# Kernel tuning notes

Hardware: AMD Instinct MI355X
Metric: run time of the kernel (lower is better)

## Reference

```python
import jax, jax.numpy as jnp
import numpy as np

N_NODES = 100000


def _graph_conv(x, W, b, src, dst, n_nodes):
    # DGL GraphConv, norm='both', weight applied before aggregation (in>out).
    E = src.shape[0]
    ones = jnp.ones((E,), dtype=x.dtype)
    out_deg = jax.ops.segment_sum(ones, src, num_segments=n_nodes)
    in_deg = jax.ops.segment_sum(ones, dst, num_segments=n_nodes)
    out_norm = jnp.clip(out_deg, 1.0, None) ** -0.5  # [N]
    in_norm = jnp.clip(in_deg, 1.0, None) ** -0.5    # [N]
    h = (x * out_norm[:, None]) @ W                  # [N, out] dense GEMM first
    msg = h[src]                                     # gather  [E, out]
    agg = jax.ops.segment_sum(msg, dst, num_segments=n_nodes)  # scatter-add
    return agg * in_norm[:, None] + b


def setup_inputs() -> dict:
    key = jax.random.key(0)
    k1, k2, k3, k4, k5 = jax.random.split(key, 5)
    E = 1600000
    features = jax.random.normal(k1, (N_NODES, 128), dtype=jnp.float32)
    src = jax.random.randint(k2, (E,), 0, N_NODES, dtype=jnp.int64)
    dst = jax.random.randint(k3, (E,), 0, N_NODES, dtype=jnp.int64)
    W1 = jax.random.normal(k4, (128, 64), dtype=jnp.float32) * (1.0 / np.sqrt(128))
    b1 = jnp.zeros((64,), dtype=jnp.float32)
    W2 = jax.random.normal(k5, (64, 32), dtype=jnp.float32) * (1.0 / np.sqrt(64))
    b2 = jnp.zeros((32,), dtype=jnp.float32)
    return {"features": features, "src": src, "dst": dst,
            "W1": W1, "b1": b1, "W2": W2, "b2": b2}


def reference(features, src, dst, W1, b1, W2, b2):
    x = jax.nn.relu(_graph_conv(features, W1, b1, src, dst, N_NODES))
    x = _graph_conv(x, W2, b2, src, dst, N_NODES)
    return x
```

## Files before the change

kernel.cpp:

```cpp
#include <hip/hip_runtime.h>
#include <hip/hip_bf16.h>


#define BSH 7
#define BNODES 128
#define SRCMASK 0x1FFFF
#define CAP 2560
#define CHUNK 4096

__device__ __forceinline__ unsigned short f2bf(float f) {
    unsigned int u = __float_as_uint(f);
    return (unsigned short)((u + 0x7FFFu + ((u >> 16) & 1u)) >> 16);
}

__device__ __forceinline__ float bflo(unsigned int u) {
    return __uint_as_float(u << 16);
}
__device__ __forceinline__ float bfhi(unsigned int u) {
    return __uint_as_float(u & 0xFFFF0000u);
}

__global__ __launch_bounds__(1024) void k_place(const int* __restrict__ src,
        const int* __restrict__ dst, int* __restrict__ ebuf,
        unsigned char* __restrict__ sbuf, int* __restrict__ offs,
        int* __restrict__ soffs, int E) {
    __shared__ int lh[800], s[800];
    int t = threadIdx.x;
    int e0 = blockIdx.x * CHUNK;
    int e1 = min(e0 + CHUNK, E);
    if (t < 800) lh[t] = 0;
    __syncthreads();
    for (int i = e0 + t; i < e1; i += 1024) {
        atomicAdd(&lh[dst[i] >> BSH], 0x10000);
        atomicAdd(&lh[src[i] >> BSH], 1);
    }
    __syncthreads();
    if (t < 800) s[t] = lh[t];
    __syncthreads();
    for (int o = 1; o < 800; o <<= 1) {
        int u = (t < 800 && t >= o) ? s[t - o] : 0;
        __syncthreads();
        if (t < 800) s[t] += u;
        __syncthreads();
    }
    int obase = blockIdx.x * 801;
    if (t < 800) {
        int incl = s[t], c = lh[t];
        int bd = (incl >> 16) - (c >> 16);
        int bs = (incl & 0xFFFF) - (c & 0xFFFF);
        offs[obase + t] = bd;
        soffs[obase + t] = bs;
        s[t] = (bd << 16) | bs;
    }
    if (t == 0) { offs[obase + 800] = e1 - e0; soffs[obase + 800] = e1 - e0; }
    __syncthreads();
    for (int i = e0 + t; i < e1; i += 1024) {
        int sv = src[i], d = dst[i];
        int pd = atomicAdd(&s[d >> BSH], 0x10000) >> 16;
        ebuf[e0 + pd] = sv | ((d & (BNODES - 1)) << 17);
        int ps = atomicAdd(&s[sv >> BSH], 1) & 0xFFFF;
        sbuf[e0 + ps] = (unsigned char)(sv & (BNODES - 1));
    }
}

__global__ __launch_bounds__(1024) void k_sort2(const int* __restrict__ ebuf,
        const unsigned char* __restrict__ sbuf, const int* __restrict__ offs,
        const int* __restrict__ soffs, int* __restrict__ csrc,
        int* __restrict__ ostart, int* __restrict__ oend,
        float* __restrict__ nI, float* __restrict__ nO, int n, int NBLK) {
    __shared__ int cnt[BNODES], cur[BNODES], s[BNODES], scnt[BNODES];
    __shared__ int segst[400], segen[400], sst[400], sen[400];
    int t = threadIdx.x, b = blockIdx.x;
    if (t < NBLK) {
        segst[t] = t * CHUNK + offs[t * 801 + b];
        segen[t] = t * CHUNK + offs[t * 801 + b + 1];
        sst[t]   = t * CHUNK + soffs[t * 801 + b];
        sen[t]   = t * CHUNK + soffs[t * 801 + b + 1];
    }
    if (t < BNODES) { cnt[t] = 0; scnt[t] = 0; }
    __syncthreads();
    int grp = t >> 3, ln = t & 7;
    for (int sg = grp; sg < NBLK; sg += 128) {
        int en = segen[sg];
        for (int i = segst[sg] + ln; i < en; i += 8)
            atomicAdd(&cnt[ebuf[i] >> 17], 1);
        int en2 = sen[sg];
        for (int i = sst[sg] + ln; i < en2; i += 8)
            atomicAdd(&scnt[sbuf[i]], 1);
    }
    __syncthreads();
    if (t < BNODES) s[t] = cnt[t];
    __syncthreads();
    for (int o = 1; o < BNODES; o <<= 1) {
        int u = (t < BNODES && t >= o) ? s[t - o] : 0;
        __syncthreads();
        if (t < BNODES) s[t] += u;
        __syncthreads();
    }
    if (t < BNODES) {
        int e0 = b * CAP;
        int st = e0 + s[t] - cnt[t];
        cur[t] = st;
        int g = b * BNODES + t;
        if (g < n) {
            ostart[g] = st;
            oend[g] = e0 + s[t];
            nI[g] = rsqrtf(fmaxf((float)cnt[t], 1.0f));
            nO[g] = rsqrtf(fmaxf((float)scnt[t], 1.0f));
        }
    }
    __syncthreads();
    for (int sg = grp; sg < NBLK; sg += 128) {
        int en = segen[sg];
        for (int i = segst[sg] + ln; i < en; i += 8) {
            int p = ebuf[i];
            int pos = atomicAdd(&cur[p >> 17], 1);
            csrc[pos] = p & SRCMASK;
        }
    }
}

__global__ __launch_bounds__(256) void k_gemm1(const float* __restrict__ x,
                        const float* __restrict__ W1, const float* __restrict__ nO,
                        unsigned short* __restrict__ h1, int n) {
    __shared__ float sX[64 * 132];
    __shared__ float sW[128 * 64];
    const int t = threadIdx.x;
    {
        const float4* W4 = (const float4*)W1;
        float4* sW4 = (float4*)sW;
#pragma unroll
        for (int i = 0; i < 8; i++) sW4[t + 256 * i] = W4[t + 256 * i];
    }
    const int rowbase = blockIdx.x * 64;
    {
        const float4* x4 = (const float4*)x;
        float4* sX4 = (float4*)sX;
#pragma unroll
        for (int i = 0; i < 8; i++) {
            int f = t + 256 * i;
            int row = f >> 5, kc = f & 31;
            int grow = rowbase + row;
            float4 v = make_float4(0.f, 0.f, 0.f, 0.f);
            if (grow < n) v = x4[(size_t)grow * 32 + kc];
            sX4[row * 33 + kc] = v;
        }
    }
    __syncthreads();
    const int lane = t & 63, wv = t >> 6;
    const int rg = lane >> 2, cg = lane & 3;
    const int c0 = wv * 16 + cg * 4;
    float acc[4][4] = {};
    for (int kk = 0; kk < 128; kk += 4) {
        float xr[4][4], wr[4][4];
#pragma unroll
        for (int i = 0; i < 4; i++)
            *(float4*)xr[i] = *(const float4*)&sX[(rg + 16 * i) * 132 + kk];
#pragma unroll
        for (int j = 0; j < 4; j++)
            *(float4*)wr[j] = *(const float4*)&sW[(kk + j) * 64 + c0];
#pragma unroll
        for (int j = 0; j < 4; j++)
#pragma unroll
            for (int i = 0; i < 4; i++)
#pragma unroll
                for (int c = 0; c < 4; c++)
                    acc[i][c] = fmaf(xr[i][j], wr[j][c], acc[i][c]);
    }
#pragma unroll
    for (int i = 0; i < 4; i++) {
        int grow = rowbase + rg + 16 * i;
        if (grow < n) {
            float nf = nO[grow];
            ushort4 o;
            o.x = f2bf(acc[i][0] * nf); o.y = f2bf(acc[i][1] * nf);
            o.z = f2bf(acc[i][2] * nf); o.w = f2bf(acc[i][3] * nf);
            *(ushort4*)&h1[(size_t)grow * 64 + c0] = o;
        }
    }
}

__global__ void k_agg64(const unsigned short* __restrict__ h,
                        const int* __restrict__ csrc,
                        const int* __restrict__ ostart, const int* __restrict__ oend,
                        const float* __restrict__ nI, const float* __restrict__ b1,
                        float* __restrict__ x2, int n) {
    int node = blockIdx.x * 4 + (threadIdx.x >> 6);
    int lane = threadIdx.x & 63;
    if (node >= n) return;
    int s0 = ostart[node], s1 = oend[node];
    int sub = lane >> 3;
    int c8 = (lane & 7) * 8;
    float a[8] = {}, d[8] = {};
    int e = s0;
    for (; e + 15 < s1; e += 16) {
        int p0 = csrc[e + sub];
        int p1 = csrc[e + 8 + sub];
        uint4 u0 = *(const uint4*)&h[(size_t)p0 * 64 + c8];
        uint4 u1 = *(const uint4*)&h[(size_t)p1 * 64 + c8];
        a[0] += bflo(u0.x); a[1] += bfhi(u0.x);
        a[2] += bflo(u0.y); a[3] += bfhi(u0.y);
        a[4] += bflo(u0.z); a[5] += bfhi(u0.z);
        a[6] += bflo(u0.w); a[7] += bfhi(u0.w);
        d[0] += bflo(u1.x); d[1] += bfhi(u1.x);
        d[2] += bflo(u1.y); d[3] += bfhi(u1.y);
        d[4] += bflo(u1.z); d[5] += bfhi(u1.z);
        d[6] += bflo(u1.w); d[7] += bfhi(u1.w);
    }
    for (; e < s1; e += 8) {
        if (e + sub < s1) {
            int p = csrc[e + sub];
            uint4 u = *(const uint4*)&h[(size_t)p * 64 + c8];
            a[0] += bflo(u.x); a[1] += bfhi(u.x);
            a[2] += bflo(u.y); a[3] += bfhi(u.y);
            a[4] += bflo(u.z); a[5] += bfhi(u.z);
            a[6] += bflo(u.w); a[7] += bfhi(u.w);
        }
    }
#pragma unroll
    for (int i = 0; i < 8; i++) a[i] += d[i];
#pragma unroll
    for (int i = 0; i < 8; i++) {
        a[i] += __shfl(a[i], lane ^ 8, 64);
        a[i] += __shfl(a[i], lane ^ 16, 64);
        a[i] += __shfl(a[i], lane ^ 32, 64);
    }
    if (sub == 0) {
        float ni = nI[node];
        float4 o0, o1;
        o0.x = fmaxf(fmaf(a[0], ni, b1[c8 + 0]), 0.f);
        o0.y = fmaxf(fmaf(a[1], ni, b1[c8 + 1]), 0.f);
        o0.z = fmaxf(fmaf(a[2], ni, b1[c8 + 2]), 0.f);
        o0.w = fmaxf(fmaf(a[3], ni, b1[c8 + 3]), 0.f);
        o1.x = fmaxf(fmaf(a[4], ni, b1[c8 + 4]), 0.f);
        o1.y = fmaxf(fmaf(a[5], ni, b1[c8 + 5]), 0.f);
        o1.z = fmaxf(fmaf(a[6], ni, b1[c8 + 6]), 0.f);
        o1.w = fmaxf(fmaf(a[7], ni, b1[c8 + 7]), 0.f);
        *(float4*)&x2[(size_t)node * 64 + c8] = o0;
        *(float4*)&x2[(size_t)node * 64 + c8 + 4] = o1;
    }
}

__global__ __launch_bounds__(256) void k_gemm2(const float* __restrict__ x2,
                        const float* __restrict__ W2, const float* __restrict__ nO,
                        unsigned short* __restrict__ h2, int n) {
    __shared__ float sX[128 * 68];
    __shared__ float sW[64 * 32];
    const int t = threadIdx.x;
    {
        const float4* W4 = (const float4*)W2;
        float4* sW4 = (float4*)sW;
#pragma unroll
        for (int i = 0; i < 2; i++) sW4[t + 256 * i] = W4[t + 256 * i];
    }
    const int rowbase = blockIdx.x * 128;
    {
        const float4* x4 = (const float4*)x2;
        float4* sX4 = (float4*)sX;
#pragma unroll
        for (int i = 0; i < 8; i++) {
            int f = t + 256 * i;
            int row = f >> 4, kc = f & 15;
            int grow = rowbase + row;
            float4 v = make_float4(0.f, 0.f, 0.f, 0.f);
            if (grow < n) v = x4[(size_t)grow * 16 + kc];
            sX4[row * 17 + kc] = v;
        }
    }
    __syncthreads();
    const int lane = t & 63, wv = t >> 6;
    const int whalf = wv >> 1, chalf = wv & 1;
    const int rg = lane >> 2, cg = lane & 3;
    const int c0 = chalf * 16 + cg * 4;
    const int rloc = whalf * 64 + rg;
    float acc[4][4] = {};
    for (int kk = 0; kk < 64; kk += 4) {
        float xr[4][4], wr[4][4];
#pragma unroll
        for (int i = 0; i < 4; i++)
            *(float4*)xr[i] = *(const float4*)&sX[(rloc + 16 * i) * 68 + kk];
#pragma unroll
        for (int j = 0; j < 4; j++)
            *(float4*)wr[j] = *(const float4*)&sW[(kk + j) * 32 + c0];
#pragma unroll
        for (int j = 0; j < 4; j++)
#pragma unroll
            for (int i = 0; i < 4; i++)
#pragma unroll
                for (int c = 0; c < 4; c++)
                    acc[i][c] = fmaf(xr[i][j], wr[j][c], acc[i][c]);
    }
#pragma unroll
    for (int i = 0; i < 4; i++) {
        int grow = rowbase + rloc + 16 * i;
        if (grow < n) {
            float nf = nO[grow];
            ushort4 o;
            o.x = f2bf(acc[i][0] * nf); o.y = f2bf(acc[i][1] * nf);
            o.z = f2bf(acc[i][2] * nf); o.w = f2bf(acc[i][3] * nf);
            *(ushort4*)&h2[(size_t)grow * 32 + c0] = o;
        }
    }
}

__global__ void k_agg32(const unsigned short* __restrict__ h,
                        const int* __restrict__ csrc,
                        const int* __restrict__ ostart, const int* __restrict__ oend,
                        const float* __restrict__ nI, const float* __restrict__ b2,
                        float* __restrict__ out, int n) {
    int node = blockIdx.x * 4 + (threadIdx.x >> 6);
    int lane = threadIdx.x & 63;
    if (node >= n) return;
    int s0 = ostart[node], s1 = oend[node];
    int sub = lane >> 2;
    int c8 = (lane & 3) * 8;
    float a[8] = {};
    int e = s0;
    for (; e + 15 < s1; e += 16) {
        int p = csrc[e + sub];
        uint4 u = *(const uint4*)&h[(size_t)p * 32 + c8];
        a[0] += bflo(u.x); a[1] += bfhi(u.x);
        a[2] += bflo(u.y); a[3] += bfhi(u.y);
        a[4] += bflo(u.z); a[5] += bfhi(u.z);
        a[6] += bflo(u.w); a[7] += bfhi(u.w);
    }
    for (; e < s1; e += 16) {
        if (e + sub < s1) {
            int p = csrc[e + sub];
            uint4 u = *(const uint4*)&h[(size_t)p * 32 + c8];
            a[0] += bflo(u.x); a[1] += bfhi(u.x);
            a[2] += bflo(u.y); a[3] += bfhi(u.y);
            a[4] += bflo(u.z); a[5] += bfhi(u.z);
            a[6] += bflo(u.w); a[7] += bfhi(u.w);
        }
    }
#pragma unroll
    for (int i = 0; i < 8; i++) {
        a[i] += __shfl(a[i], lane ^ 4, 64);
        a[i] += __shfl(a[i], lane ^ 8, 64);
        a[i] += __shfl(a[i], lane ^ 16, 64);
        a[i] += __shfl(a[i], lane ^ 32, 64);
    }
    if (sub == 0) {
        float ni = nI[node];
        float4 o0, o1;
        o0.x = fmaf(a[0], ni, b2[c8 + 0]);
        o0.y = fmaf(a[1], ni, b2[c8 + 1]);
        o0.z = fmaf(a[2], ni, b2[c8 + 2]);
        o0.w = fmaf(a[3], ni, b2[c8 + 3]);
        o1.x = fmaf(a[4], ni, b2[c8 + 4]);
        o1.y = fmaf(a[5], ni, b2[c8 + 5]);
        o1.z = fmaf(a[6], ni, b2[c8 + 6]);
        o1.w = fmaf(a[7], ni, b2[c8 + 7]);
        *(float4*)&out[(size_t)node * 32 + c8] = o0;
        *(float4*)&out[(size_t)node * 32 + c8 + 4] = o1;
    }
}

extern "C" void kernel_launch(void* const* d_in, const int* in_sizes, int n_in,
                              void* d_out, int out_size, void* d_ws, size_t ws_size,
                              hipStream_t stream) {
    const float* x   = (const float*)d_in[0];
    const int*   src = (const int*)d_in[1];
    const int*   dst = (const int*)d_in[2];
    const float* W1  = (const float*)d_in[3];
    const float* b1  = (const float*)d_in[4];
    const float* W2  = (const float*)d_in[5];
    const float* b2  = (const float*)d_in[6];
    float* out = (float*)d_out;

    const int N = in_sizes[0] / 128;
    const int E = in_sizes[1];
    const int NB = (N + BNODES - 1) / BNODES;
    const int NBLK = (E + CHUNK - 1) / CHUNK;

    char* wsb = (char*)d_ws;
    float* nO     = (float*)wsb;  wsb += (size_t)N * 4;
    float* nI     = (float*)wsb;  wsb += (size_t)N * 4;
    int*   ostart = (int*)wsb;    wsb += (size_t)N * 4;
    int*   oend   = (int*)wsb;    wsb += (size_t)N * 4;
    int*   csrc   = (int*)wsb;    wsb += (size_t)NB * CAP * 4;
    int*   offs   = (int*)wsb;    wsb += (size_t)NBLK * 801 * 4;
    unsigned short* h1 = (unsigned short*)wsb;
                                  wsb += (size_t)N * 64 * 2;
    float* x2     = (float*)wsb;  wsb += (size_t)N * 64 * 4;
    unsigned short* h2 = h1;
    int*   ebuf   = (int*)x2;
    unsigned char* sbuf = (unsigned char*)(ebuf) + (size_t)E * 4;
    int*   soffs  = (int*)(sbuf + (size_t)E);

    k_place<<<NBLK, 1024, 0, stream>>>(src, dst, ebuf, sbuf, offs, soffs, E);
    k_sort2<<<NB, 1024, 0, stream>>>(ebuf, sbuf, offs, soffs, csrc,
                                     ostart, oend, nI, nO, N, NBLK);

    k_gemm1<<<(N + 63) / 64, 256, 0, stream>>>(x, W1, nO, h1, N);
    k_agg64<<<(N + 3) / 4, 256, 0, stream>>>(h1, csrc, ostart, oend, nI, b1, x2, N);

    k_gemm2<<<(N + 127) / 128, 256, 0, stream>>>(x2, W2, nO, h2, N);
    k_agg32<<<(N + 3) / 4, 256, 0, stream>>>(h2, csrc, ostart, oend, nI, b2, out, N);
}
```

Measured before the change: 293.7 us.

## Split layer-1 features into four column slabs for cache-friendly aggregation

Gemm1 now writes h1 as four planar 16-column bf16 slabs instead of interleaved 64-wide rows. The layer-1 aggregation is split into four passes, one per slab, so each gathered working set (~3.2MB) fits in cache rather than the full 12.8MB table. Each wave handles 8 nodes with 16 edges in flight, and x2 is stored slab-major with gemm2 reading it accordingly. In exchange, the edge index lists are read four times and more shuffle reductions are done per node.

```diff
diff --git a/kernel.cpp b/kernel.cpp
--- a/kernel.cpp
+++ b/kernel.cpp
@@ -167,6 +167,7 @@
                 for (int c = 0; c < 4; c++)
                     acc[i][c] = fmaf(xr[i][j], wr[j][c], acc[i][c]);
     }
+    const size_t pl = (size_t)n * 16;
 #pragma unroll
     for (int i = 0; i < 4; i++) {
         int grow = rowbase + rg + 16 * i;
@@ -175,69 +176,64 @@
             ushort4 o;
             o.x = f2bf(acc[i][0] * nf); o.y = f2bf(acc[i][1] * nf);
             o.z = f2bf(acc[i][2] * nf); o.w = f2bf(acc[i][3] * nf);
-            *(ushort4*)&h1[(size_t)grow * 64 + c0] = o;
-        }
-    }
-}
-
-__global__ void k_agg64(const unsigned short* __restrict__ h,
-                        const int* __restrict__ csrc,
-                        const int* __restrict__ ostart, const int* __restrict__ oend,
-                        const float* __restrict__ nI, const float* __restrict__ b1,
-                        float* __restrict__ x2, int n) {
-    int node = blockIdx.x * 4 + (threadIdx.x >> 6);
-    int lane = threadIdx.x & 63;
-    if (node >= n) return;
-    int s0 = ostart[node], s1 = oend[node];
-    int sub = lane >> 3;
-    int c8 = (lane & 7) * 8;
-    float a[8] = {}, d[8] = {};
-    int e = s0;
-    for (; e + 15 < s1; e += 16) {
-        int p0 = csrc[e + sub];
-        int p1 = csrc[e + 8 + sub];
-        uint4 u0 = *(const uint4*)&h[(size_t)p0 * 64 + c8];
-        uint4 u1 = *(const uint4*)&h[(size_t)p1 * 64 + c8];
-        a[0] += bflo(u0.x); a[1] += bfhi(u0.x);
-        a[2] += bflo(u0.y); a[3] += bfhi(u0.y);
-        a[4] += bflo(u0.z); a[5] += bfhi(u0.z);
-        a[6] += bflo(u0.w); a[7] += bfhi(u0.w);
-        d[0] += bflo(u1.x); d[1] += bfhi(u1.x);
-        d[2] += bflo(u1.y); d[3] += bfhi(u1.y);
-        d[4] += bflo(u1.z); d[5] += bfhi(u1.z);
-        d[6] += bflo(u1.w); d[7] += bfhi(u1.w);
-    }
-    for (; e < s1; e += 8) {
-        if (e + sub < s1) {
-            int p = csrc[e + sub];
-            uint4 u = *(const uint4*)&h[(size_t)p * 64 + c8];
-            a[0] += bflo(u.x); a[1] += bfhi(u.x);
-            a[2] += bflo(u.y); a[3] += bfhi(u.y);
-            a[4] += bflo(u.z); a[5] += bfhi(u.z);
-            a[6] += bflo(u.w); a[7] += bfhi(u.w);
-        }
-    }
-#pragma unroll
-    for (int i = 0; i < 8; i++) a[i] += d[i];
-#pragma unroll
-    for (int i = 0; i < 8; i++) {
-        a[i] += __shfl(a[i], lane ^ 8, 64);
-        a[i] += __shfl(a[i], lane ^ 16, 64);
-        a[i] += __shfl(a[i], lane ^ 32, 64);
-    }
-    if (sub == 0) {
-        float ni = nI[node];
-        float4 o0, o1;
-        o0.x = fmaxf(fmaf(a[0], ni, b1[c8 + 0]), 0.f);
-        o0.y = fmaxf(fmaf(a[1], ni, b1[c8 + 1]), 0.f);
-        o0.z = fmaxf(fmaf(a[2], ni, b1[c8 + 2]), 0.f);
-        o0.w = fmaxf(fmaf(a[3], ni, b1[c8 + 3]), 0.f);
-        o1.x = fmaxf(fmaf(a[4], ni, b1[c8 + 4]), 0.f);
-        o1.y = fmaxf(fmaf(a[5], ni, b1[c8 + 5]), 0.f);
-        o1.z = fmaxf(fmaf(a[6], ni, b1[c8 + 6]), 0.f);
-        o1.w = fmaxf(fmaf(a[7], ni, b1[c8 + 7]), 0.f);
-        *(float4*)&x2[(size_t)node * 64 + c8] = o0;
-        *(float4*)&x2[(size_t)node * 64 + c8 + 4] = o1;
+            *(ushort4*)&h1[(size_t)wv * pl + (size_t)grow * 16 + cg * 4] = o;
+        }
+    }
+}
+
+__global__ __launch_bounds__(256) void k_agg64s2(const unsigned short* __restrict__ h,
+        const int* __restrict__ csrc, const int* __restrict__ ostart,
+        const int* __restrict__ oend, const float* __restrict__ nI,
+        const float* __restrict__ b1, float* __restrict__ x2, int n) {
+    const int s  = blockIdx.x & 3;
+    const int nb = blockIdx.x >> 2;
+    const int wid = threadIdx.x >> 6, lane = threadIdx.x & 63;
+    const int node0 = nb * 32 + wid * 8;
+    if (node0 >= n) return;
+    const int sub = lane >> 2;
+    const int cl = lane & 3;
+    const uint2* hs = (const uint2*)(h + (size_t)s * n * 16);
+    float* x2s = x2 + (size_t)s * n * 16;
+    const float4 bb = *(const float4*)&b1[s * 16 + cl * 4];
+    int pre = min(node0 + (lane & 7), n - 1);
+    int sA = ostart[pre], sB = oend[pre];
+#pragma unroll
+    for (int g = 0; g < 8; g++) {
+        int node = node0 + g;
+        if (node >= n) break;
+        int s0 = __shfl(sA, g, 64), s1 = __shfl(sB, g, 64);
+        float a0 = 0.f, a1 = 0.f, a2 = 0.f, a3 = 0.f;
+        for (int e = s0 + sub; e < s1; e += 16) {
+            int p = csrc[e];
+            uint2 u = hs[(size_t)p * 4 + cl];
+            a0 += bflo(u.x); a1 += bfhi(u.x);
+            a2 += bflo(u.y); a3 += bfhi(u.y);
+        }
+        a0 += __shfl(a0, lane ^ 4, 64);
+        a1 += __shfl(a1, lane ^ 4, 64);
+        a2 += __shfl(a2, lane ^ 4, 64);
+        a3 += __shfl(a3, lane ^ 4, 64);
+        a0 += __shfl(a0, lane ^ 8, 64);
+        a1 += __shfl(a1, lane ^ 8, 64);
+        a2 += __shfl(a2, lane ^ 8, 64);
+        a3 += __shfl(a3, lane ^ 8, 64);
+        a0 += __shfl(a0, lane ^ 16, 64);
+        a1 += __shfl(a1, lane ^ 16, 64);
+        a2 += __shfl(a2, lane ^ 16, 64);
+        a3 += __shfl(a3, lane ^ 16, 64);
+        a0 += __shfl(a0, lane ^ 32, 64);
+        a1 += __shfl(a1, lane ^ 32, 64);
+        a2 += __shfl(a2, lane ^ 32, 64);
+        a3 += __shfl(a3, lane ^ 32, 64);
+        if (sub == 0) {
+            float ni = nI[node];
+            float4 o;
+            o.x = fmaxf(fmaf(a0, ni, bb.x), 0.f);
+            o.y = fmaxf(fmaf(a1, ni, bb.y), 0.f);
+            o.z = fmaxf(fmaf(a2, ni, bb.z), 0.f);
+            o.w = fmaxf(fmaf(a3, ni, bb.w), 0.f);
+            *(float4*)&x2s[(size_t)node * 16 + cl * 4] = o;
+        }
     }
 }
 
@@ -254,6 +250,7 @@
         for (int i = 0; i < 2; i++) sW4[t + 256 * i] = W4[t + 256 * i];
     }
     const int rowbase = blockIdx.x * 128;
+    const size_t n4 = (size_t)n * 4;
     {
         const float4* x4 = (const float4*)x2;
         float4* sX4 = (float4*)sX;
@@ -263,7 +260,8 @@
             int row = f >> 4, kc = f & 15;
             int grow = rowbase + row;
             float4 v = make_float4(0.f, 0.f, 0.f, 0.f);
-            if (grow < n) v = x4[(size_t)grow * 16 + kc];
+            if (grow < n)
+                v = x4[(size_t)(kc >> 2) * n4 + (size_t)grow * 4 + (kc & 3)];
             sX4[row * 17 + kc] = v;
         }
     }
@@ -394,7 +392,8 @@
                                      ostart, oend, nI, nO, N, NBLK);
 
     k_gemm1<<<(N + 63) / 64, 256, 0, stream>>>(x, W1, nO, h1, N);
-    k_agg64<<<(N + 3) / 4, 256, 0, stream>>>(h1, csrc, ostart, oend, nI, b1, x2, N);
+    k_agg64s2<<<((N + 31) / 32) * 4, 256, 0, stream>>>(h1, csrc, ostart, oend,
+                                                       nI, b1, x2, N);
 
     k_gemm2<<<(N + 127) / 128, 256, 0, stream>>>(x2, W2, nO, h2, N);
     k_agg32<<<(N + 3) / 4, 256, 0, stream>>>(h2, csrc, ostart, oend, nI, b2, out, N);
```

Measured after the change: 333.2 us. 1.13x slower.

## Fuse layer-2 GEMM into layer-1 aggregation epilogue

Applied to the files above, without the earlier changes.

The first aggregation kernel now applies bias and ReLU, then multiplies each node's 64-wide row by W2 (held transposed in shared memory) with a shuffle reduction, and writes the bf16 h2 directly. This removes the fp32 x2 intermediate write and read and one kernel launch. In exchange every 4-node block reloads W2 into shared memory, which adds a barrier and extra shuffles per node. The workspace layout is reshuffled so that h2 aliases the sort scratch buffer.

```diff
diff --git a/kernel.cpp b/kernel.cpp
--- a/kernel.cpp
+++ b/kernel.cpp
@@ -180,17 +180,28 @@
     }
 }
 
-__global__ void k_agg64(const unsigned short* __restrict__ h,
-                        const int* __restrict__ csrc,
-                        const int* __restrict__ ostart, const int* __restrict__ oend,
-                        const float* __restrict__ nI, const float* __restrict__ b1,
-                        float* __restrict__ x2, int n) {
+__global__ __launch_bounds__(256) void k_agg64g2(const unsigned short* __restrict__ h,
+        const int* __restrict__ csrc,
+        const int* __restrict__ ostart, const int* __restrict__ oend,
+        const float* __restrict__ nI, const float* __restrict__ nO,
+        const float* __restrict__ b1, const float* __restrict__ W2,
+        unsigned short* __restrict__ h2, int n) {
+    __shared__ float sWT[32 * 68];
+    {
+        int t = threadIdx.x;
+        for (int i = t; i < 2048; i += 256) {
+            int cc = i & 31, k = i >> 5;
+            sWT[cc * 68 + k] = W2[(size_t)k * 32 + cc];
+        }
+    }
+    __syncthreads();
     int node = blockIdx.x * 4 + (threadIdx.x >> 6);
     int lane = threadIdx.x & 63;
     if (node >= n) return;
     int s0 = ostart[node], s1 = oend[node];
     int sub = lane >> 3;
-    int c8 = (lane & 7) * 8;
+    int q = lane & 7;
+    int c8 = q * 8;
     float a[8] = {}, d[8] = {};
     int e = s0;
     for (; e + 15 < s1; e += 16) {
@@ -225,81 +236,40 @@
         a[i] += __shfl(a[i], lane ^ 16, 64);
         a[i] += __shfl(a[i], lane ^ 32, 64);
     }
-    if (sub == 0) {
-        float ni = nI[node];
-        float4 o0, o1;
-        o0.x = fmaxf(fmaf(a[0], ni, b1[c8 + 0]), 0.f);
-        o0.y = fmaxf(fmaf(a[1], ni, b1[c8 + 1]), 0.f);
-        o0.z = fmaxf(fmaf(a[2], ni, b1[c8 + 2]), 0.f);
-        o0.w = fmaxf(fmaf(a[3], ni, b1[c8 + 3]), 0.f);
-        o1.x = fmaxf(fmaf(a[4], ni, b1[c8 + 4]), 0.f);
-        o1.y = fmaxf(fmaf(a[5], ni, b1[c8 + 5]), 0.f);
-        o1.z = fmaxf(fmaf(a[6], ni, b1[c8 + 6]), 0.f);
-        o1.w = fmaxf(fmaf(a[7], ni, b1[c8 + 7]), 0.f);
-        *(float4*)&x2[(size_t)node * 64 + c8] = o0;
-        *(float4*)&x2[(size_t)node * 64 + c8 + 4] = o1;
-    }
-}
-
-__global__ __launch_bounds__(256) void k_gemm2(const float* __restrict__ x2,
-                        const float* __restrict__ W2, const float* __restrict__ nO,
-                        unsigned short* __restrict__ h2, int n) {
-    __shared__ float sX[128 * 68];
-    __shared__ float sW[64 * 32];
-    const int t = threadIdx.x;
-    {
-        const float4* W4 = (const float4*)W2;
-        float4* sW4 = (float4*)sW;
-#pragma unroll
-        for (int i = 0; i < 2; i++) sW4[t + 256 * i] = W4[t + 256 * i];
-    }
-    const int rowbase = blockIdx.x * 128;
-    {
-        const float4* x4 = (const float4*)x2;
-        float4* sX4 = (float4*)sX;
-#pragma unroll
-        for (int i = 0; i < 8; i++) {
-            int f = t + 256 * i;
-            int row = f >> 4, kc = f & 15;
-            int grow = rowbase + row;
-            float4 v = make_float4(0.f, 0.f, 0.f, 0.f);
-            if (grow < n) v = x4[(size_t)grow * 16 + kc];
-            sX4[row * 17 + kc] = v;
-        }
-    }
-    __syncthreads();
-    const int lane = t & 63, wv = t >> 6;
-    const int whalf = wv >> 1, chalf = wv & 1;
-    const int rg = lane >> 2, cg = lane & 3;
-    const int c0 = chalf * 16 + cg * 4;
-    const int rloc = whalf * 64 + rg;
-    float acc[4][4] = {};
-    for (int kk = 0; kk < 64; kk += 4) {
-        float xr[4][4], wr[4][4];
-#pragma unroll
-        for (int i = 0; i < 4; i++)
-            *(float4*)xr[i] = *(const float4*)&sX[(rloc + 16 * i) * 68 + kk];
-#pragma unroll
-        for (int j = 0; j < 4; j++)
-            *(float4*)wr[j] = *(const float4*)&sW[(kk + j) * 32 + c0];
-#pragma unroll
-        for (int j = 0; j < 4; j++)
-#pragma unroll
-            for (int i = 0; i < 4; i++)
-#pragma unroll
-                for (int c = 0; c < 4; c++)
-                    acc[i][c] = fmaf(xr[i][j], wr[j][c], acc[i][c]);
-    }
-#pragma unroll
-    for (int i = 0; i < 4; i++) {
-        int grow = rowbase + rloc + 16 * i;
-        if (grow < n) {
-            float nf = nO[grow];
-            ushort4 o;
-            o.x = f2bf(acc[i][0] * nf); o.y = f2bf(acc[i][1] * nf);
-            o.z = f2bf(acc[i][2] * nf); o.w = f2bf(acc[i][3] * nf);
-            *(ushort4*)&h2[(size_t)grow * 32 + c0] = o;
-        }
+    float ni = nI[node];
+    float v[8];
+#pragma unroll
+    for (int i = 0; i < 8; i++)
+        v[i] = fmaxf(fmaf(a[i], ni, b1[c8 + i]), 0.f);
+    float p4[4];
+#pragma unroll
+    for (int c = 0; c < 4; c++) {
+        const float* wr = &sWT[(sub * 4 + c) * 68 + c8];
+        float4 wlo = *(const float4*)&wr[0];
+        float4 whi = *(const float4*)&wr[4];
+        float pc;
+        pc = v[0] * wlo.x;
+        pc = fmaf(v[1], wlo.y, pc);
+        pc = fmaf(v[2], wlo.z, pc);
+        pc = fmaf(v[3], wlo.w, pc);
+        pc = fmaf(v[4], whi.x, pc);
+        pc = fmaf(v[5], whi.y, pc);
+        pc = fmaf(v[6], whi.z, pc);
+        pc = fmaf(v[7], whi.w, pc);
+        p4[c] = pc;
+    }
+#pragma unroll
+    for (int c = 0; c < 4; c++) {
+        p4[c] += __shfl(p4[c], lane ^ 1, 64);
+        p4[c] += __shfl(p4[c], lane ^ 2, 64);
+        p4[c] += __shfl(p4[c], lane ^ 4, 64);
+    }
+    if (q == 0) {
+        float nOv = nO[node];
+        ushort4 o;
+        o.x = f2bf(p4[0] * nOv); o.y = f2bf(p4[1] * nOv);
+        o.z = f2bf(p4[2] * nOv); o.w = f2bf(p4[3] * nOv);
+        *(ushort4*)&h2[(size_t)node * 32 + sub * 4] = o;
     }
 }
 
@@ -383,19 +353,19 @@
     int*   offs   = (int*)wsb;    wsb += (size_t)NBLK * 801 * 4;
     unsigned short* h1 = (unsigned short*)wsb;
                                   wsb += (size_t)N * 64 * 2;
-    float* x2     = (float*)wsb;  wsb += (size_t)N * 64 * 4;
-    unsigned short* h2 = h1;
-    int*   ebuf   = (int*)x2;
-    unsigned char* sbuf = (unsigned char*)(ebuf) + (size_t)E * 4;
-    int*   soffs  = (int*)(sbuf + (size_t)E);
+    char*  scr    = wsb;          wsb += (size_t)E * 4 + E + (size_t)NBLK * 801 * 4;
+    int*   ebuf   = (int*)scr;
+    unsigned char* sbuf = (unsigned char*)scr + (size_t)E * 4;
+    int*   soffs  = (int*)((char*)scr + (size_t)E * 4 + E);
+    unsigned short* h2 = (unsigned short*)scr;
 
     k_place<<<NBLK, 1024, 0, stream>>>(src, dst, ebuf, sbuf, offs, soffs, E);
     k_sort2<<<NB, 1024, 0, stream>>>(ebuf, sbuf, offs, soffs, csrc,
                                      ostart, oend, nI, nO, N, NBLK);
 
     k_gemm1<<<(N + 63) / 64, 256, 0, stream>>>(x, W1, nO, h1, N);
-    k_agg64<<<(N + 3) / 4, 256, 0, stream>>>(h1, csrc, ostart, oend, nI, b1, x2, N);
-
-    k_gemm2<<<(N + 127) / 128, 256, 0, stream>>>(x2, W2, nO, h2, N);
+    k_agg64g2<<<(N + 3) / 4, 256, 0, stream>>>(h1, csrc, ostart, oend,
+                                               nI, nO, b1, W2, h2, N);
+
     k_agg32<<<(N + 3) / 4, 256, 0, stream>>>(h2, csrc, ostart, oend, nI, b2, out, N);
 }
```

Result: slower. 305.1 us (+3.9%).
